# Kernel tuning notes

Measured on AMD Instinct MI355X. Metric: run time of the kernel, lower is better.

The kernel has to match this reference:

```python
import jax, jax.numpy as jnp
import numpy as np

N_QUBITS = 10
Q_DEPTH = 6


def _apply_1q(state, gate, wire):
    """Apply a 2x2 gate (or batched [B,2,2] gates) to `wire` of state [B,2,...,2]."""
    s = jnp.moveaxis(state, wire + 1, -1)
    if gate.ndim == 2:
        s = s @ gate.T  # new_j = sum_i G[j,i] * old_i
    else:
        s = jnp.einsum('b...i,bji->b...j', s, gate)
    return jnp.moveaxis(s, -1, wire + 1)


def _apply_cnot(state, ctrl, tgt):
    s = jnp.moveaxis(state, (ctrl + 1, tgt + 1), (-2, -1))
    s = jnp.stack([s[..., 0, :], s[..., 1, ::-1]], axis=-2)  # flip target where ctrl=1
    return jnp.moveaxis(s, (-2, -1), (ctrl + 1, tgt + 1))


def _ry(theta):
    """RY(theta) = [[cos(t/2), -sin(t/2)], [sin(t/2), cos(t/2)]]; theta scalar or [B]."""
    c, s = jnp.cos(theta / 2.0), jnp.sin(theta / 2.0)
    return jnp.stack([jnp.stack([c, -s], -1), jnp.stack([s, c], -1)], -2)


def _vqc(angles, q_weights):
    """angles: [B, n_qubits] per-sample RY angles; q_weights: [q_depth, n_qubits].
    Returns <PauliZ_w> for every wire: [B, n_qubits]. All gates are real -> float32 state."""
    B, n = angles.shape
    q_depth = q_weights.shape[0]
    # H-layer on |0...0> gives the uniform superposition: all amplitudes 2^{-n/2}
    state = jnp.full((B,) + (2,) * n, 2.0 ** (-n / 2.0), dtype=angles.dtype)
    # RY layer with per-sample input angles
    for w in range(n):
        state = _apply_1q(state, _ry(angles[:, w]), w)
    # q_depth x (brick-wall CNOT entangler + trainable RY layer)
    for k in range(q_depth):
        for i in range(0, n - 1, 2):
            state = _apply_cnot(state, i, i + 1)
        for i in range(1, n - 1, 2):
            state = _apply_cnot(state, i, i + 1)
        for w in range(n):
            state = _apply_1q(state, _ry(q_weights[k, w]), w)
    # expval(PauliZ(w)) = P(wire w = 0) - P(wire w = 1)
    probs = state * state  # real statevector
    exps = []
    for w in range(n):
        p = jnp.moveaxis(probs, w + 1, 1).reshape(B, 2, -1).sum(-1)
        exps.append(p[:, 0] - p[:, 1])
    return jnp.stack(exps, -1)


def setup_inputs() -> dict:
    key = jax.random.key(0)
    ks = jax.random.split(key, 6)
    B, D_IN, OUT = 8192, 512, 64
    x = jax.random.normal(ks[0], (B, D_IN), dtype=jnp.float32)
    W1 = jax.random.normal(ks[1], (D_IN, N_QUBITS), dtype=jnp.float32) * (1.0 / np.sqrt(D_IN))
    b1 = jnp.zeros((N_QUBITS,), dtype=jnp.float32)
    # keras 'uniform' initializer: U(-0.05, 0.05)
    q_weights = jax.random.uniform(ks[2], (Q_DEPTH, N_QUBITS), dtype=jnp.float32,
                                   minval=-0.05, maxval=0.05)
    W2 = jax.random.normal(ks[3], (N_QUBITS, OUT), dtype=jnp.float32) * (1.0 / np.sqrt(N_QUBITS))
    b2 = jnp.zeros((OUT,), dtype=jnp.float32)
    return {"x": x, "W1": W1, "b1": b1, "q_weights": q_weights, "W2": W2, "b2": b2}


def reference(x, W1, b1, q_weights, W2, b2):
    # Dense(n_qubits, tanh) then scale to angles in (-pi/2, pi/2)
    angles = jnp.tanh(x @ W1 + b1) * (jnp.pi / 2.0)  # [B, n_qubits]
    q_out = _vqc(angles, q_weights)                   # [B, n_qubits]
    return q_out @ W2 + b2                            # [B, output_dim]
```

## Files before the change

### kernel.cpp

```cpp
#include <hip/hip_runtime.h>

#define NQ 10
#define QD 6
#define DIN 512
#define DOUT 64

template <int CTRL>
__device__ __forceinline__ float dppf(float v) {
    return __int_as_float(__builtin_amdgcn_mov_dpp(__float_as_int(v), CTRL, 0xF, 0xF, true));
}
template <int M>
__device__ __forceinline__ float sx(float v) {
    if constexpr (M == 1)      return dppf<0xB1>(v);
    else if constexpr (M == 2) return dppf<0x4E>(v);
    else return __int_as_float(__builtin_amdgcn_ds_swizzle(__float_as_int(v), (M << 10) | 0x1F));
}
__device__ __forceinline__ float red16(float v) {
    v += sx<8>(v); v += sx<4>(v); v += sx<2>(v); v += sx<1>(v);
    return v;
}

__global__ __launch_bounds__(256) void dqc_main(
    const float* __restrict__ x,
    const float* __restrict__ W1,
    const float* __restrict__ b1,
    const float* __restrict__ qw,
    const float* __restrict__ W2,
    const float* __restrict__ b2,
    float* __restrict__ out,
    const int B)
{
    __shared__ __align__(16) float csl[2 * QD * NQ];

    const int tid = threadIdx.x;
    if (tid < QD * NQ) {
        float s, c;
        sincosf(qw[tid] * 0.5f, &s, &c);
        csl[2 * tid] = c; csl[2 * tid + 1] = s;
    }

    const int lane16 = tid & 15;
    const int b  = (blockIdx.x * 256 + tid) >> 4;
    const int bb = (b < B) ? b : (B - 1);

    float xr[32];
    {
        const float4* xp = (const float4*)(x + (size_t)bb * DIN + lane16 * 32);
        #pragma unroll
        for (int i = 0; i < 8; ++i) {
            const float4 v = xp[i];
            xr[4*i] = v.x; xr[4*i+1] = v.y; xr[4*i+2] = v.z; xr[4*i+3] = v.w;
        }
    }
    float dot[NQ];
    #pragma unroll
    for (int w = 0; w < NQ; ++w) dot[w] = 0.f;
    {
        const float4* wp = (const float4*)(W1 + (size_t)lane16 * 32 * NQ);
        #pragma unroll
        for (int j = 0; j < 16; ++j) {
            const float4 f0 = wp[5*j], f1 = wp[5*j+1], f2 = wp[5*j+2],
                         f3 = wp[5*j+3], f4 = wp[5*j+4];
            const float xa = xr[2*j], xb = xr[2*j+1];
            dot[0]=fmaf(xa,f0.x,dot[0]); dot[1]=fmaf(xa,f0.y,dot[1]);
            dot[2]=fmaf(xa,f0.z,dot[2]); dot[3]=fmaf(xa,f0.w,dot[3]);
            dot[4]=fmaf(xa,f1.x,dot[4]); dot[5]=fmaf(xa,f1.y,dot[5]);
            dot[6]=fmaf(xa,f1.z,dot[6]); dot[7]=fmaf(xa,f1.w,dot[7]);
            dot[8]=fmaf(xa,f2.x,dot[8]); dot[9]=fmaf(xa,f2.y,dot[9]);
            dot[0]=fmaf(xb,f2.z,dot[0]); dot[1]=fmaf(xb,f2.w,dot[1]);
            dot[2]=fmaf(xb,f3.x,dot[2]); dot[3]=fmaf(xb,f3.y,dot[3]);
            dot[4]=fmaf(xb,f3.z,dot[4]); dot[5]=fmaf(xb,f3.w,dot[5]);
            dot[6]=fmaf(xb,f4.x,dot[6]); dot[7]=fmaf(xb,f4.y,dot[7]);
            dot[8]=fmaf(xb,f4.z,dot[8]); dot[9]=fmaf(xb,f4.w,dot[9]);
        }
    }
    #pragma unroll
    for (int w = 0; w < NQ; ++w) dot[w] = red16(dot[w]);

    float u0[NQ], u1[NQ];
    #pragma unroll
    for (int w = 0; w < NQ; ++w) {
        const float th2 = tanhf(dot[w] + b1[w]) * 0.78539816339744830962f;
        float s, c;
        sincosf(th2, &s, &c);
        const float isq2 = 0.70710678118654752440f;
        u0[w] = (c - s) * isq2;
        u1[w] = (c + s) * isq2;
    }

    float a[64];
    {
        float lf = ((lane16 & 8) ? u1[0] : u0[0]);
        lf *= ((lane16 & 4) ? u1[1] : u0[1]);
        lf *= ((lane16 & 2) ? u1[2] : u0[2]);
        lf *= ((lane16 & 1) ? u1[3] : u0[3]);
        a[0] = lf;
        #pragma unroll
        for (int w = 4; w < NQ; ++w) {
            const int n = 1 << (w - 4);
            #pragma unroll
            for (int i = n - 1; i >= 0; --i) {
                const float base = a[i];
                a[2*i]   = base * u0[w];
                a[2*i+1] = base * u1[w];
            }
        }
    }

    __syncthreads();

    #pragma unroll 1
    for (int k = 0; k < QD; ++k) {
        const float4* cp = (const float4*)(csl + k * 2 * NQ);
        const float4 q0 = cp[0], q1 = cp[1], q2 = cp[2], q3 = cp[3], q4 = cp[4];
        const float C0=q0.x,S0=q0.y, C1=q0.z,S1=q0.w;
        const float C2=q1.x,S2=q1.y, C3=q1.z,S3=q1.w;
        const float C4=q2.x,S4=q2.y, C5=q2.z,S5=q2.w;
        const float C6=q3.x,S6=q3.y, C7=q3.z,S7=q3.w;
        const float C8=q4.x,S8=q4.y, C9=q4.z,S9=q4.w;

        {
            const bool cb = (lane16 & 8) != 0;
            #pragma unroll
            for (int r = 0; r < 64; ++r) { const float v = sx<4>(a[r]); a[r] = cb ? v : a[r]; }
        }
        {
            const bool cb = (lane16 & 2) != 0;
            #pragma unroll
            for (int r = 0; r < 64; ++r) { const float v = sx<1>(a[r]); a[r] = cb ? v : a[r]; }
        }
        {
            #pragma unroll
            for (int i = 0; i < 16; ++i) { const float t = a[32+i]; a[32+i] = a[48+i]; a[48+i] = t; }
        }
        {
            #pragma unroll
            for (int j = 0; j < 4; ++j)
                #pragma unroll
                for (int i = 0; i < 4; ++i) { const int r = 16*j + 8 + i; const float t = a[r]; a[r] = a[r+4]; a[r+4] = t; }
        }
        {
            #pragma unroll
            for (int r = 2; r < 64; r += 4) { const float t = a[r]; a[r] = a[r+1]; a[r+1] = t; }
        }
        {
            const bool cb = (lane16 & 4) != 0;
            #pragma unroll
            for (int r = 0; r < 64; ++r) { const float v = sx<2>(a[r]); a[r] = cb ? v : a[r]; }
        }
        {
            #pragma unroll
            for (int j = 0; j < 2; ++j)
                #pragma unroll
                for (int i = 0; i < 8; ++i) { const int r = 32*j + 16 + i; const float t = a[r]; a[r] = a[r+8]; a[r+8] = t; }
        }
        {
            #pragma unroll
            for (int r = 0; r < 64; r += 8) {
                float t = a[r+4]; a[r+4] = a[r+6]; a[r+6] = t;
                t = a[r+5]; a[r+5] = a[r+7]; a[r+7] = t;
            }
        }
        {
            const bool cb = (lane16 & 1) != 0;
            const float al = cb ? -S4 :  C4;
            const float be = cb ?  C4 : -S4;
            const float ga = cb ?  C4 :  S4;
            const float de = cb ?  S4 :  C4;
            #pragma unroll
            for (int r = 0; r < 32; ++r) {
                const float a0 = a[r], a1 = a[r+32];
                a[r]    = fmaf(al, a0, be * a1);
                a[r+32] = fmaf(ga, a0, de * a1);
            }
        }
        {   const float ss = (lane16 & 8) ? S0 : -S0;
            #pragma unroll
            for (int r = 0; r < 64; ++r) { const float p = sx<8>(a[r]); a[r] = fmaf(C0, a[r], ss * p); }
        }
        {   const float ss = (lane16 & 4) ? S1 : -S1;
            #pragma unroll
            for (int r = 0; r < 64; ++r) { const float p = sx<4>(a[r]); a[r] = fmaf(C1, a[r], ss * p); }
        }
        {   const float ss = (lane16 & 2) ? S2 : -S2;
            #pragma unroll
            for (int r = 0; r < 64; ++r) { const float p = sx<2>(a[r]); a[r] = fmaf(C2, a[r], ss * p); }
        }
        {   const float ss = (lane16 & 1) ? S3 : -S3;
            #pragma unroll
            for (int r = 0; r < 64; ++r) { const float p = sx<1>(a[r]); a[r] = fmaf(C3, a[r], ss * p); }
        }
        {
            #pragma unroll
            for (int r = 0; r < 64; ++r) if (!(r & 16)) {
                const float a0 = a[r], a1 = a[r|16];
                a[r]    = fmaf(C5, a0, -(S5 * a1));
                a[r|16] = fmaf(C5, a1,  S5 * a0);
            }
        }
        {
            #pragma unroll
            for (int r = 0; r < 64; ++r) if (!(r & 8)) {
                const float a0 = a[r], a1 = a[r|8];
                a[r]   = fmaf(C6, a0, -(S6 * a1));
                a[r|8] = fmaf(C6, a1,  S6 * a0);
            }
        }
        {
            #pragma unroll
            for (int r = 0; r < 64; ++r) if (!(r & 4)) {
                const float a0 = a[r], a1 = a[r|4];
                a[r]   = fmaf(C7, a0, -(S7 * a1));
                a[r|4] = fmaf(C7, a1,  S7 * a0);
            }
        }
        {
            #pragma unroll
            for (int r = 0; r < 64; ++r) if (!(r & 2)) {
                const float a0 = a[r], a1 = a[r|2];
                a[r]   = fmaf(C8, a0, -(S8 * a1));
                a[r|2] = fmaf(C8, a1,  S8 * a0);
            }
        }
        {
            #pragma unroll
            for (int r = 0; r < 64; ++r) if (!(r & 1)) {
                const float a0 = a[r], a1 = a[r|1];
                a[r]   = fmaf(C9, a0, -(S9 * a1));
                a[r|1] = fmaf(C9, a1,  S9 * a0);
            }
        }
    }

    float tot = 0.f, t4 = 0.f, t5 = 0.f, t6 = 0.f, t7 = 0.f, t8 = 0.f, t9 = 0.f;
    #pragma unroll
    for (int r = 0; r < 64; ++r) {
        const float p = a[r] * a[r];
        tot += p;
        if (r & 32) t4 += p;
        if (r & 16) t5 += p;
        if (r & 8)  t6 += p;
        if (r & 4)  t7 += p;
        if (r & 2)  t8 += p;
        if (r & 1)  t9 += p;
    }
    float e[NQ];
    e[0] = (lane16 & 8) ? -tot : tot;
    e[1] = (lane16 & 4) ? -tot : tot;
    e[2] = (lane16 & 2) ? -tot : tot;
    e[3] = (lane16 & 1) ? -tot : tot;
    e[4] = tot - 2.f * t4;
    e[5] = tot - 2.f * t5;
    e[6] = tot - 2.f * t6;
    e[7] = tot - 2.f * t7;
    e[8] = tot - 2.f * t8;
    e[9] = tot - 2.f * t9;
    #pragma unroll
    for (int w = 0; w < NQ; ++w) e[w] = red16(e[w]);

    if (b < B) {
        float4 o = ((const float4*)b2)[lane16];
        #pragma unroll
        for (int w = 0; w < NQ; ++w) {
            const float4 wv = ((const float4*)(W2 + w * DOUT))[lane16];
            o.x = fmaf(e[w], wv.x, o.x);
            o.y = fmaf(e[w], wv.y, o.y);
            o.z = fmaf(e[w], wv.z, o.z);
            o.w = fmaf(e[w], wv.w, o.w);
        }
        ((float4*)(out + (size_t)b * DOUT))[lane16] = o;
    }
}

extern "C" void kernel_launch(void* const* d_in, const int* in_sizes, int n_in,
                              void* d_out, int out_size, void* d_ws, size_t ws_size,
                              hipStream_t stream) {
    const float* x  = (const float*)d_in[0];
    const float* W1 = (const float*)d_in[1];
    const float* b1 = (const float*)d_in[2];
    const float* qw = (const float*)d_in[3];
    const float* W2 = (const float*)d_in[4];
    const float* b2 = (const float*)d_in[5];
    float* out = (float*)d_out;

    const int B = in_sizes[0] / DIN;
    const int blocks = (B + 15) / 16;
    dqc_main<<<blocks, 256, 0, stream>>>(x, W1, b1, qw, W2, b2, out, B);
}
```

Baseline: 121.0 us.

## Fold CNOT permutations into relabeled basis and use packed float2 FMA

```diff
diff --git a/kernel.cpp b/kernel.cpp
--- a/kernel.cpp
+++ b/kernel.cpp
@@ -4,6 +4,12 @@
 #define QD 6
 #define DIN 512
 #define DOUT 64
+
+typedef float v2f __attribute__((ext_vector_type(2)));
+
+__device__ __forceinline__ v2f sp(float s) { v2f r; r.x = s; r.y = s; return r; }
+__device__ __forceinline__ v2f mk(float a, float b) { v2f r; r.x = a; r.y = b; return r; }
+#define PKF(a, b, c) __builtin_elementwise_fma(a, b, c)
 
 template <int CTRL>
 __device__ __forceinline__ float dppf(float v) {
@@ -15,12 +21,14 @@
     else if constexpr (M == 2) return dppf<0x4E>(v);
     else return __int_as_float(__builtin_amdgcn_ds_swizzle(__float_as_int(v), (M << 10) | 0x1F));
 }
+template <int M>
+__device__ __forceinline__ v2f sx2(v2f v) { return mk(sx<M>(v.x), sx<M>(v.y)); }
 __device__ __forceinline__ float red16(float v) {
     v += sx<8>(v); v += sx<4>(v); v += sx<2>(v); v += sx<1>(v);
     return v;
 }
 
-__global__ __launch_bounds__(256) void dqc_main(
+__global__ __launch_bounds__(256, 2) void dqc_main(
     const float* __restrict__ x,
     const float* __restrict__ W1,
     const float* __restrict__ b1,
@@ -88,22 +96,21 @@
         u1[w] = (c + s) * isq2;
     }
 
-    float a[64];
+    v2f A[32];
     {
         float lf = ((lane16 & 8) ? u1[0] : u0[0]);
-        lf *= ((lane16 & 4) ? u1[1] : u0[1]);
+        lf *= ((((lane16 >> 2) ^ (lane16 >> 3)) & 1) ? u1[1] : u0[1]);
         lf *= ((lane16 & 2) ? u1[2] : u0[2]);
-        lf *= ((lane16 & 1) ? u1[3] : u0[3]);
-        a[0] = lf;
-        #pragma unroll
-        for (int w = 4; w < NQ; ++w) {
-            const int n = 1 << (w - 4);
-            #pragma unroll
-            for (int i = n - 1; i >= 0; --i) {
-                const float base = a[i];
-                a[2*i]   = base * u0[w];
-                a[2*i+1] = base * u1[w];
-            }
+        lf *= (((lane16 ^ (lane16 >> 1)) & 1) ? u1[3] : u0[3]);
+        #pragma unroll
+        for (int m = 0; m < 32; ++m) {
+            float f = ((m & 16) ? u1[4] : u0[4]);
+            f *= ((((m >> 3) ^ (m >> 4)) & 1) ? u1[5] : u0[5]);
+            f *= ((m & 4) ? u1[6] : u0[6]);
+            f *= ((((m >> 1) ^ (m >> 2)) & 1) ? u1[7] : u0[7]);
+            f *= ((m & 1) ? u1[8] : u0[8]);
+            f *= lf;
+            A[m] = (m & 1) ? mk(f * u1[9], f * u0[9]) : mk(f * u0[9], f * u1[9]);
         }
     }
 
@@ -112,149 +119,147 @@
     #pragma unroll 1
     for (int k = 0; k < QD; ++k) {
         const float4* cp = (const float4*)(csl + k * 2 * NQ);
-        const float4 q0 = cp[0], q1 = cp[1], q2 = cp[2], q3 = cp[3], q4 = cp[4];
-        const float C0=q0.x,S0=q0.y, C1=q0.z,S1=q0.w;
-        const float C2=q1.x,S2=q1.y, C3=q1.z,S3=q1.w;
-        const float C4=q2.x,S4=q2.y, C5=q2.z,S5=q2.w;
-        const float C6=q3.x,S6=q3.y, C7=q3.z,S7=q3.w;
-        const float C8=q4.x,S8=q4.y, C9=q4.z,S9=q4.w;
-
-        {
-            const bool cb = (lane16 & 8) != 0;
-            #pragma unroll
-            for (int r = 0; r < 64; ++r) { const float v = sx<4>(a[r]); a[r] = cb ? v : a[r]; }
-        }
-        {
-            const bool cb = (lane16 & 2) != 0;
-            #pragma unroll
-            for (int r = 0; r < 64; ++r) { const float v = sx<1>(a[r]); a[r] = cb ? v : a[r]; }
-        }
-        {
-            #pragma unroll
-            for (int i = 0; i < 16; ++i) { const float t = a[32+i]; a[32+i] = a[48+i]; a[48+i] = t; }
-        }
-        {
-            #pragma unroll
-            for (int j = 0; j < 4; ++j)
-                #pragma unroll
-                for (int i = 0; i < 4; ++i) { const int r = 16*j + 8 + i; const float t = a[r]; a[r] = a[r+4]; a[r+4] = t; }
-        }
-        {
-            #pragma unroll
-            for (int r = 2; r < 64; r += 4) { const float t = a[r]; a[r] = a[r+1]; a[r+1] = t; }
-        }
-        {
+        const float4 g0 = cp[0], g1 = cp[1], g2 = cp[2], g3 = cp[3], g4 = cp[4];
+        const float C0=g0.x,S0=g0.y, C1=g0.z,S1=g0.w;
+        const float C2=g1.x,S2=g1.y, C3=g1.z,S3=g1.w;
+        const float C4=g2.x,S4=g2.y, C5=g2.z,S5=g2.w;
+        const float C6=g3.x,S6=g3.y, C7=g3.z,S7=g3.w;
+        const float C8=g4.x,S8=g4.y, C9=g4.z,S9=g4.w;
+        const bool fuse = (k < QD - 1);
+
+        {
+            const float g = (lane16 & 8) ? S0 : -S0;
+            const v2f al = sp(C0), be = sp(g);
+            #pragma unroll
+            for (int m = 0; m < 32; ++m) { const v2f p = sx2<8>(A[m]); A[m] = PKF(al, A[m], be * p); }
+        }
+        {
+            const float g = (lane16 & 2) ? S2 : -S2;
             const bool cb = (lane16 & 4) != 0;
-            #pragma unroll
-            for (int r = 0; r < 64; ++r) { const float v = sx<2>(a[r]); a[r] = cb ? v : a[r]; }
-        }
-        {
-            #pragma unroll
-            for (int j = 0; j < 2; ++j)
-                #pragma unroll
-                for (int i = 0; i < 8; ++i) { const int r = 32*j + 16 + i; const float t = a[r]; a[r] = a[r+8]; a[r+8] = t; }
-        }
-        {
-            #pragma unroll
-            for (int r = 0; r < 64; r += 8) {
-                float t = a[r+4]; a[r+4] = a[r+6]; a[r+6] = t;
-                t = a[r+5]; a[r+5] = a[r+7]; a[r+7] = t;
-            }
+            const v2f al = sp(cb ? g : C2), be = sp(cb ? C2 : g);
+            #pragma unroll
+            for (int m = 0; m < 32; ++m) { const v2f p = sx2<2>(A[m]); A[m] = PKF(al, A[m], be * p); }
         }
         {
             const bool cb = (lane16 & 1) != 0;
-            const float al = cb ? -S4 :  C4;
-            const float be = cb ?  C4 : -S4;
-            const float ga = cb ?  C4 :  S4;
-            const float de = cb ?  S4 :  C4;
-            #pragma unroll
-            for (int r = 0; r < 32; ++r) {
-                const float a0 = a[r], a1 = a[r+32];
-                a[r]    = fmaf(al, a0, be * a1);
-                a[r+32] = fmaf(ga, a0, de * a1);
-            }
-        }
-        {   const float ss = (lane16 & 8) ? S0 : -S0;
-            #pragma unroll
-            for (int r = 0; r < 64; ++r) { const float p = sx<8>(a[r]); a[r] = fmaf(C0, a[r], ss * p); }
-        }
-        {   const float ss = (lane16 & 4) ? S1 : -S1;
-            #pragma unroll
-            for (int r = 0; r < 64; ++r) { const float p = sx<4>(a[r]); a[r] = fmaf(C1, a[r], ss * p); }
-        }
-        {   const float ss = (lane16 & 2) ? S2 : -S2;
-            #pragma unroll
-            for (int r = 0; r < 64; ++r) { const float p = sx<2>(a[r]); a[r] = fmaf(C2, a[r], ss * p); }
-        }
-        {   const float ss = (lane16 & 1) ? S3 : -S3;
-            #pragma unroll
-            for (int r = 0; r < 64; ++r) { const float p = sx<1>(a[r]); a[r] = fmaf(C3, a[r], ss * p); }
-        }
-        {
-            #pragma unroll
-            for (int r = 0; r < 64; ++r) if (!(r & 16)) {
-                const float a0 = a[r], a1 = a[r|16];
-                a[r]    = fmaf(C5, a0, -(S5 * a1));
-                a[r|16] = fmaf(C5, a1,  S5 * a0);
-            }
-        }
-        {
-            #pragma unroll
-            for (int r = 0; r < 64; ++r) if (!(r & 8)) {
-                const float a0 = a[r], a1 = a[r|8];
-                a[r]   = fmaf(C6, a0, -(S6 * a1));
-                a[r|8] = fmaf(C6, a1,  S6 * a0);
-            }
-        }
-        {
-            #pragma unroll
-            for (int r = 0; r < 64; ++r) if (!(r & 4)) {
-                const float a0 = a[r], a1 = a[r|4];
-                a[r]   = fmaf(C7, a0, -(S7 * a1));
-                a[r|4] = fmaf(C7, a1,  S7 * a0);
-            }
-        }
-        {
-            #pragma unroll
-            for (int r = 0; r < 64; ++r) if (!(r & 2)) {
-                const float a0 = a[r], a1 = a[r|2];
-                a[r]   = fmaf(C8, a0, -(S8 * a1));
-                a[r|2] = fmaf(C8, a1,  S8 * a0);
-            }
-        }
-        {
-            #pragma unroll
-            for (int r = 0; r < 64; ++r) if (!(r & 1)) {
-                const float a0 = a[r], a1 = a[r|1];
-                a[r]   = fmaf(C9, a0, -(S9 * a1));
-                a[r|1] = fmaf(C9, a1,  S9 * a0);
-            }
-        }
-    }
-
-    float tot = 0.f, t4 = 0.f, t5 = 0.f, t6 = 0.f, t7 = 0.f, t8 = 0.f, t9 = 0.f;
-    #pragma unroll
-    for (int r = 0; r < 64; ++r) {
-        const float p = a[r] * a[r];
-        tot += p;
-        if (r & 32) t4 += p;
-        if (r & 16) t5 += p;
-        if (r & 8)  t6 += p;
-        if (r & 4)  t7 += p;
-        if (r & 2)  t8 += p;
-        if (r & 1)  t9 += p;
-    }
+            const v2f a0 = sp(cb ? -S4 : C4), b0 = sp(cb ? C4 : -S4);
+            const v2f a1 = sp(cb ?  S4 : C4), b1v = sp(cb ? C4 :  S4);
+            #pragma unroll
+            for (int m = 0; m < 16; ++m) {
+                const v2f lo = A[m], hi = A[m + 16];
+                A[m]      = PKF(a0, lo, b0 * hi);
+                A[m + 16] = PKF(a1, hi, b1v * lo);
+            }
+        }
+        {
+            #pragma unroll
+            for (int m = 0; m < 32; ++m) {
+                if (m & 4) continue;
+                const v2f lo = A[m], hi = A[m + 4];
+                if ((m >> 3) & 1) {
+                    A[m]     = PKF(sp(-S6), lo, sp(C6) * hi);
+                    A[m + 4] = PKF(sp( S6), hi, sp(C6) * lo);
+                } else {
+                    A[m]     = PKF(sp(C6), lo, sp(-S6) * hi);
+                    A[m + 4] = PKF(sp(C6), hi, sp( S6) * lo);
+                }
+            }
+        }
+        {
+            #pragma unroll
+            for (int q = 0; q < 16; ++q) {
+                const v2f lo = A[2*q], hi = A[2*q+1];
+                if (q & 1) {
+                    A[2*q]   = PKF(sp(-S8), lo, sp(C8) * hi);
+                    A[2*q+1] = PKF(sp( S8), hi, sp(C8) * lo);
+                } else {
+                    A[2*q]   = PKF(sp(C8), lo, sp(-S8) * hi);
+                    A[2*q+1] = PKF(sp(C8), hi, sp( S8) * lo);
+                }
+            }
+        }
+
+        {
+            const float g = (lane16 & 4) ? S1 : -S1;
+            const bool cb = fuse && ((lane16 & 8) != 0);
+            const v2f al = sp(cb ? -g : C1), be = sp(cb ? C1 : g);
+            #pragma unroll
+            for (int m = 0; m < 32; ++m) { const v2f p = sx2<4>(A[m]); A[m] = PKF(al, A[m], be * p); }
+        }
+        {
+            const float g = (lane16 & 1) ? S3 : -S3;
+            const bool cb = fuse && ((lane16 & 2) != 0);
+            const v2f al = sp(cb ? -g : C3), be = sp(cb ? C3 : g);
+            #pragma unroll
+            for (int m = 0; m < 32; ++m) { const v2f p = sx2<1>(A[m]); A[m] = PKF(al, A[m], be * p); }
+        }
+        {
+            const float a0c = fuse ?  S5 : C5,  b0c = fuse ? C5 : -S5;
+            const float a1c = fuse ? -S5 : C5,  b1c = fuse ? C5 :  S5;
+            #pragma unroll
+            for (int m = 0; m < 32; ++m) {
+                if (m & 8) continue;
+                const v2f lo = A[m], hi = A[m + 8];
+                if ((m >> 4) & 1) {
+                    A[m]     = PKF(sp(a0c), lo, sp(b0c) * hi);
+                    A[m + 8] = PKF(sp(a1c), hi, sp(b1c) * lo);
+                } else {
+                    A[m]     = PKF(sp(C5), lo, sp(-S5) * hi);
+                    A[m + 8] = PKF(sp(C5), hi, sp( S5) * lo);
+                }
+            }
+        }
+        {
+            const float a0c = fuse ?  S7 : C7,  b0c = fuse ? C7 : -S7;
+            const float a1c = fuse ? -S7 : C7,  b1c = fuse ? C7 :  S7;
+            #pragma unroll
+            for (int m = 0; m < 32; ++m) {
+                if (m & 2) continue;
+                const v2f lo = A[m], hi = A[m + 2];
+                if ((m >> 2) & 1) {
+                    A[m]     = PKF(sp(a0c), lo, sp(b0c) * hi);
+                    A[m + 2] = PKF(sp(a1c), hi, sp(b1c) * lo);
+                } else {
+                    A[m]     = PKF(sp(C7), lo, sp(-S7) * hi);
+                    A[m + 2] = PKF(sp(C7), hi, sp( S7) * lo);
+                }
+            }
+        }
+        {
+            const v2f Ae = sp(C9), Be = mk(-S9, S9);
+            const v2f Ao = fuse ? mk(S9, -S9) : Ae;
+            const v2f Bo = fuse ? sp(C9) : Be;
+            #pragma unroll
+            for (int m = 0; m < 32; ++m) {
+                const v2f s = mk(A[m].y, A[m].x);
+                A[m] = (m & 1) ? PKF(Ao, A[m], Bo * s) : PKF(Ae, A[m], Be * s);
+            }
+        }
+    }
+
+    v2f tot2 = sp(0.f), q4 = sp(0.f), q5 = sp(0.f), q6 = sp(0.f), q7 = sp(0.f), q8 = sp(0.f);
+    #pragma unroll
+    for (int m = 0; m < 32; ++m) {
+        const v2f P = A[m] * A[m];
+        tot2 += P;
+        if (m & 16) q4 += P;
+        if (m & 8)  q5 += P;
+        if (m & 4)  q6 += P;
+        if (m & 2)  q7 += P;
+        if (m & 1)  q8 += P;
+    }
+    const float tot = tot2.x + tot2.y;
     float e[NQ];
     e[0] = (lane16 & 8) ? -tot : tot;
     e[1] = (lane16 & 4) ? -tot : tot;
     e[2] = (lane16 & 2) ? -tot : tot;
     e[3] = (lane16 & 1) ? -tot : tot;
-    e[4] = tot - 2.f * t4;
-    e[5] = tot - 2.f * t5;
-    e[6] = tot - 2.f * t6;
-    e[7] = tot - 2.f * t7;
-    e[8] = tot - 2.f * t8;
-    e[9] = tot - 2.f * t9;
+    e[4] = tot - 2.f * (q4.x + q4.y);
+    e[5] = tot - 2.f * (q5.x + q5.y);
+    e[6] = tot - 2.f * (q6.x + q6.y);
+    e[7] = tot - 2.f * (q7.x + q7.y);
+    e[8] = tot - 2.f * (q8.x + q8.y);
+    e[9] = tot - 2.f * tot2.y;
     #pragma unroll
     for (int w = 0; w < NQ; ++w) e[w] = red16(e[w]);
 
```

Measured after the change: 115.6 us. 4.5% less time.
